# Performance work log

Measured on AMD Instinct MI355X. Metric: run time of the kernel, lower is better.

The kernel has to match this reference:

```python
import jax, jax.numpy as jnp
import numpy as np

HS, NH, HD = 768, 12, 64
MLP_DIM = 3072
WS = 14            # window size
B, H, W = 8, 64, 64
EPS = 1e-6


def _ln(x, g, b):
    mu = jnp.mean(x, axis=-1, keepdims=True)
    var = jnp.mean(jnp.square(x - mu), axis=-1, keepdims=True)
    return (x - mu) * jax.lax.rsqrt(var + EPS) * g + b


def setup_inputs() -> dict:
    key = jax.random.key(0)
    ks = jax.random.split(key, 8)
    s = 0.02
    return {
        "x": jax.random.normal(ks[0], (B, H, W, HS), dtype=jnp.float32),
        "ln1_g": jnp.ones((HS,), jnp.float32),
        "ln1_b": jnp.zeros((HS,), jnp.float32),
        "qkv_w": jax.random.normal(ks[1], (HS, 3 * HS), jnp.float32) * s,
        "qkv_b": jnp.zeros((3 * HS,), jnp.float32),
        "proj_w": jax.random.normal(ks[2], (HS, HS), jnp.float32) * s,
        "proj_b": jnp.zeros((HS,), jnp.float32),
        "rel_pos_h": jax.random.normal(ks[3], (2 * WS - 1, HD), jnp.float32) * s,
        "rel_pos_w": jax.random.normal(ks[4], (2 * WS - 1, HD), jnp.float32) * s,
        "ln2_g": jnp.ones((HS,), jnp.float32),
        "ln2_b": jnp.zeros((HS,), jnp.float32),
        "mlp_w1": jax.random.normal(ks[5], (HS, MLP_DIM), jnp.float32) * s,
        "mlp_b1": jnp.zeros((MLP_DIM,), jnp.float32),
        "mlp_w2": jax.random.normal(ks[6], (MLP_DIM, HS), jnp.float32) * s,
        "mlp_b2": jnp.zeros((HS,), jnp.float32),
    }


def reference(x, ln1_g, ln1_b, qkv_w, qkv_b, proj_w, proj_b,
              rel_pos_h, rel_pos_w, ln2_g, ln2_b,
              mlp_w1, mlp_b1, mlp_w2, mlp_b2):
    b, h, w, c = x.shape
    shortcut = x
    y = _ln(x, ln1_g, ln1_b)

    # ---- window partition (pad H,W to multiple of WS) ----
    pad = (-h) % WS
    hp = h + pad
    y = jnp.pad(y, ((0, 0), (0, pad), (0, pad), (0, 0)))
    n = hp // WS  # windows per side
    y = y.reshape(b, n, WS, n, WS, c).transpose(0, 1, 3, 2, 4, 5)
    y = y.reshape(b * n * n, WS, WS, c)          # (Bw, 14, 14, C)
    bw = y.shape[0]
    tok = WS * WS                                 # 196

    # ---- attention with decomposed relative position bias ----
    qkv = y.reshape(bw, tok, c) @ qkv_w + qkv_b   # (Bw, 196, 3C)
    qkv = qkv.reshape(bw, tok, 3, NH, HD).transpose(2, 0, 3, 1, 4)
    qkv = qkv.reshape(3, bw * NH, tok, HD)
    q, k, v = qkv[0], qkv[1], qkv[2]
    scale = HD ** -0.5
    attn = jnp.einsum('bqd,bkd->bqk', q * scale, k)  # (Bw*NH, 196, 196)

    idx = jnp.arange(WS)[:, None] - jnp.arange(WS)[None, :] + (WS - 1)
    Rh = rel_pos_h[idx]                            # (14, 14, HD)
    Rw = rel_pos_w[idx]                            # (14, 14, HD)
    qr = q.reshape(bw * NH, WS, WS, HD)
    rel_h = jnp.einsum('bhwc,hkc->bhwk', qr, Rh)   # (Bnh, h, w, k_h)
    rel_w = jnp.einsum('bhwc,wkc->bhwk', qr, Rw)   # (Bnh, h, w, k_w)
    bias = (rel_h[:, :, :, :, None] + rel_w[:, :, :, None, :])
    attn = attn + bias.reshape(bw * NH, tok, tok)

    attn = jax.nn.softmax(attn, axis=-1)
    out = jnp.einsum('bqk,bkd->bqd', attn, v)      # (Bw*NH, 196, HD)
    out = out.reshape(bw, NH, WS, WS, HD).transpose(0, 2, 3, 1, 4)
    out = out.reshape(bw, WS, WS, c) @ proj_w + proj_b

    # ---- window unpartition + crop ----
    out = out.reshape(b, n, n, WS, WS, c).transpose(0, 1, 3, 2, 4, 5)
    out = out.reshape(b, hp, hp, c)[:, :h, :w, :]

    x = shortcut + out

    # ---- MLP block ----
    y2 = _ln(x, ln2_g, ln2_b)
    y2 = jax.nn.gelu(y2 @ mlp_w1 + mlp_b1, approximate=False) @ mlp_w2 + mlp_b2
    return x + y2
```

## Files before the change

kernel.cpp:

```cpp
#include <hip/hip_runtime.h>
#include <hip/hip_bf16.h>
#include <math.h>


#define HS 768
#define NHEADS 12
#define HD 64
#define WSZ 14
#define TOK 196
#define HWDIM 64
#define NSIDE 5
#define WIN_PER_B 25

typedef __attribute__((ext_vector_type(8))) short short8;
typedef __attribute__((ext_vector_type(4))) float floatx4;
typedef __attribute__((ext_vector_type(4))) unsigned short ushort4v;

__device__ __forceinline__ float bf2f(unsigned short u) {
    union { unsigned int i; float f; } w; w.i = ((unsigned int)u) << 16; return w.f;
}
__device__ __forceinline__ unsigned short f2bu(float f) {
    __hip_bfloat16 h = __float2bfloat16(f);
    return *(unsigned short*)&h;
}

__device__ __forceinline__ void gload16(const void* g, void* l) {
    __builtin_amdgcn_global_load_lds(
        (const __attribute__((address_space(1))) void*)g,
        (__attribute__((address_space(3))) void*)l, 16, 0, 0);
}

__device__ __forceinline__ int gather_src(int m, int M, int win_base) {
    if (m >= M) return -1;
    int lwin = m / TOK, tok = m - lwin * TOK;
    int win = win_base + lwin;
    int bb = win / WIN_PER_B, r = win - bb * WIN_PER_B;
    int wi = r / NSIDE, wj = r - wi * NSIDE;
    int ti = tok / WSZ, tj = tok - ti * WSZ;
    int h = wi * WSZ + ti, w = wj * WSZ + tj;
    if (h < HWDIM && w < HWDIM) return (bb * HWDIM + h) * HWDIM + w;
    return -1;
}

__global__ __launch_bounds__(256)
void cvt_t_k(const float* __restrict__ src, __hip_bfloat16* __restrict__ dst,
             int K, int N) {
    __shared__ float t[32][33];
    int n0 = blockIdx.x * 32, k0 = blockIdx.y * 32;
    int tc = threadIdx.x & 31, tr8 = threadIdx.x >> 5;
    #pragma unroll
    for (int i = 0; i < 4; ++i) {
        int r = tr8 + i * 8;
        t[r][tc] = src[(size_t)(k0 + r) * N + n0 + tc];
    }
    __syncthreads();
    #pragma unroll
    for (int i = 0; i < 4; ++i) {
        int r = tr8 + i * 8;
        dst[(size_t)(n0 + r) * K + k0 + tc] = __float2bfloat16(t[tc][r]);
    }
}

__global__ __launch_bounds__(256)
void ln_k(const float* __restrict__ x, const float* __restrict__ g,
          const float* __restrict__ b, __hip_bfloat16* __restrict__ y) {
    int wave = threadIdx.x >> 6, lane = threadIdx.x & 63;
    int row = blockIdx.x * 4 + wave;
    const float4* xr = (const float4*)(x + (size_t)row * HS);
    float4 a0 = xr[lane], a1 = xr[lane + 64], a2 = xr[lane + 128];
    float s = a0.x + a0.y + a0.z + a0.w + a1.x + a1.y + a1.z + a1.w
            + a2.x + a2.y + a2.z + a2.w;
    float q = a0.x*a0.x + a0.y*a0.y + a0.z*a0.z + a0.w*a0.w
            + a1.x*a1.x + a1.y*a1.y + a1.z*a1.z + a1.w*a1.w
            + a2.x*a2.x + a2.y*a2.y + a2.z*a2.z + a2.w*a2.w;
    #pragma unroll
    for (int off = 32; off > 0; off >>= 1) {
        s += __shfl_down(s, off, 64);
        q += __shfl_down(q, off, 64);
    }
    s = __shfl(s, 0, 64);
    q = __shfl(q, 0, 64);
    float mu = s * (1.0f / HS);
    float var = q * (1.0f / HS) - mu * mu;
    float rstd = rsqrtf(var + 1e-6f);
    const float4* g4 = (const float4*)g;
    const float4* b4 = (const float4*)b;
    unsigned short* yr = (unsigned short*)y + (size_t)row * HS;
    float4 av[3] = {a0, a1, a2};
    #pragma unroll
    for (int c = 0; c < 3; ++c) {
        float4 gv = g4[lane + 64 * c], bv = b4[lane + 64 * c];
        float4 a = av[c];
        ushort4v o;
        o[0] = f2bu((a.x - mu) * rstd * gv.x + bv.x);
        o[1] = f2bu((a.y - mu) * rstd * gv.y + bv.y);
        o[2] = f2bu((a.z - mu) * rstd * gv.z + bv.z);
        o[3] = f2bu((a.w - mu) * rstd * gv.w + bv.w);
        *(ushort4v*)&yr[(lane + 64 * c) * 4] = o;
    }
}

template<int EP, int AGATHER, int BM, int BN, int KSPLIT>
__global__ __launch_bounds__(256, 4)
void gemm_k(const __hip_bfloat16* __restrict__ A,
            const __hip_bfloat16* __restrict__ Bt,
            const float* __restrict__ bias,
            int M, int N, int K,
            __hip_bfloat16* __restrict__ oq, __hip_bfloat16* __restrict__ okk,
            __hip_bfloat16* __restrict__ ov,
            float* __restrict__ of, const float* __restrict__ resid,
            __hip_bfloat16* __restrict__ oh,
            int win_base, int m_base)
{
    constexpr int LPW = (BM + BN) / 64;
    constexpr int FI = BM / 32;
    constexpr int FJ = BN / 32;
    constexpr int ASZ = BM * 32;
    constexpr int BSZ = BN * 32;
    __shared__ __align__(16) unsigned short lds[4 * (ASZ + BSZ)];
    unsigned short* Asb = lds;
    unsigned short* Bsb = lds + 4 * ASZ;

    int tid = threadIdx.x;
    int wave = tid >> 6, lane = tid & 63;
    int n16 = lane & 15, quad = lane >> 4;
    int wrr = wave >> 1, wcc = wave & 1;
    int bm = blockIdx.y * BM;
    int bn = blockIdx.x * BN;
    int kz = (KSPLIT > 1) ? blockIdx.z : 0;
    int kseg = K / KSPLIT;

    int srow = tid >> 2;
    int q4 = tid & 3;
    int skoff = (q4 ^ ((srow >> 1) & 3)) << 3;

    const unsigned short* Au = (const unsigned short*)A;
    const unsigned short* Bu = (const unsigned short*)Bt;

    int src0 = 0, src1 = 0;
    if (AGATHER) {
        int s0 = gather_src(bm + srow, M, win_base);
        src0 = s0 >= 0 ? s0 : 0;
        if (BM == 128) {
            int s1 = gather_src(bm + 64 + srow, M, win_base);
            src1 = s1 >= 0 ? s1 : 0;
        }
    } else {
        int m0 = bm + srow;
        src0 = m0 < M ? m0 : 0;
        if (BM == 128) { int m1 = bm + 64 + srow; src1 = m1 < M ? m1 : 0; }
    }

    const unsigned short* ap0 = Au + (size_t)src0 * K + kz * kseg + skoff;
    const unsigned short* ap1 = Au + (size_t)src1 * K + kz * kseg + skoff;
    const unsigned short* bp0 = Bu + (size_t)(bn + srow) * K + kz * kseg + skoff;
    const unsigned short* bp1 = Bu + (size_t)(bn + 64 + srow) * K + kz * kseg + skoff;

    auto stage = [&](int kt, int b) {
        size_t ko = (size_t)kt * 32;
        gload16(ap0 + ko, Asb + b * ASZ + wave * 512);
        if constexpr (BM == 128) gload16(ap1 + ko, Asb + b * ASZ + 2048 + wave * 512);
        gload16(bp0 + ko, Bsb + b * BSZ + wave * 512);
        if constexpr (BN == 128) gload16(bp1 + ko, Bsb + b * BSZ + 2048 + wave * 512);
    };

    floatx4 acc[FI][FJ] = {};
    int xr = (n16 >> 1) & 3;
    int nt = kseg >> 5;

    stage(0, 0);
    if (nt > 1) stage(1, 1);
    if (nt > 2) stage(2, 2);

    for (int t = 0; t < nt; ++t) {
        int cur = t & 3;
        int ahead = nt - 1 - t;
        if (ahead >= 2) {
            if constexpr (LPW == 4)      asm volatile("s_waitcnt vmcnt(8)" ::: "memory");
            else if constexpr (LPW == 3) asm volatile("s_waitcnt vmcnt(6)" ::: "memory");
            else                         asm volatile("s_waitcnt vmcnt(4)" ::: "memory");
        } else if (ahead == 1) {
            if constexpr (LPW == 4)      asm volatile("s_waitcnt vmcnt(4)" ::: "memory");
            else if constexpr (LPW == 3) asm volatile("s_waitcnt vmcnt(3)" ::: "memory");
            else                         asm volatile("s_waitcnt vmcnt(2)" ::: "memory");
        } else {
            asm volatile("s_waitcnt vmcnt(0)" ::: "memory");
        }
        __builtin_amdgcn_s_barrier();
        if (t + 3 < nt) stage(t + 3, (t + 3) & 3);
        short8 af[FI], bf[FJ];
        #pragma unroll
        for (int i = 0; i < FI; ++i) {
            int ra = wrr * (BM / 2) + i * 16 + n16;
            af[i] = *(const short8*)&Asb[cur * ASZ + ra * 32 + ((quad ^ xr) << 3)];
        }
        #pragma unroll
        for (int j = 0; j < FJ; ++j) {
            int rb = wcc * (BN / 2) + j * 16 + n16;
            bf[j] = *(const short8*)&Bsb[cur * BSZ + rb * 32 + ((quad ^ xr) << 3)];
        }
        #pragma unroll
        for (int i = 0; i < FI; ++i)
            #pragma unroll
            for (int j = 0; j < FJ; ++j)
                acc[i][j] = __builtin_amdgcn_mfma_f32_16x16x32_bf16(
                    af[i], bf[j], acc[i][j], 0, 0, 0);
        asm volatile("s_waitcnt lgkmcnt(0)" ::: "memory");
    }

    int rbase = bm + wrr * (BM / 2) + quad * 4;
    int cbase = bn + wcc * (BN / 2) + n16;

    if constexpr (EP == 0 || EP == 2) {
        constexpr int CLD = BN + 8;
        __syncthreads();
        unsigned short* Cs = lds;
        int ruseW[FI * 4];
        if (EP == 0) {
            #pragma unroll
            for (int i = 0; i < FI; ++i)
                #pragma unroll
                for (int r = 0; r < 4; ++r)
                    ruseW[i * 4 + r] = gather_src(rbase + i * 16 + r, M, win_base) >= 0;
        }
        #pragma unroll
        for (int j = 0; j < FJ; ++j) {
            int col_l = wcc * (BN / 2) + j * 16 + n16;
            float bcol = bias[bn + col_l];
            #pragma unroll
            for (int i = 0; i < FI; ++i) {
                #pragma unroll
                for (int r = 0; r < 4; ++r) {
                    int row_l = wrr * (BM / 2) + i * 16 + quad * 4 + r;
                    float val = acc[i][j][r] + bcol;
                    float vv;
                    if (EP == 0) {
                        vv = ruseW[i * 4 + r] ? val : bcol;
                    } else {
                        vv = 0.5f * val * (1.0f + erff(val * 0.70710678118654752f));
                    }
                    Cs[row_l * CLD + col_l] = f2bu(vv);
                }
            }
        }
        __syncthreads();
        #pragma unroll
        for (int rep = 0; rep < (BM * (BN / 64)) / 256; ++rep) {
            int idx = rep * 256 + tid;
            int row_l = idx / (BN / 64);
            int half = idx - row_l * (BN / 64);
            int m = bm + row_l;
            if (m < M) {
                unsigned short* srcu = &Cs[row_l * CLD + half * 64];
                unsigned short* dstu;
                if (EP == 0) {
                    int lwin = m / TOK, tok = m - lwin * TOK;
                    int colg = bn + half * 64;
                    int which = colg / HS;
                    int head = (colg - which * HS) >> 6;
                    __hip_bfloat16* dstp = (which == 0) ? oq : ((which == 1) ? okk : ov);
                    dstu = (unsigned short*)dstp +
                           ((size_t)(lwin * NHEADS + head) * TOK + tok) * HD;
                } else {
                    dstu = (unsigned short*)oh + (size_t)m * N + bn + half * 64;
                }
                #pragma unroll
                for (int s = 0; s < 8; ++s)
                    *(uint4*)(dstu + s * 8) = *(const uint4*)(srcu + s * 8);
            }
        }
    } else {
        int rowoff[FI * 4];
        int ruse[FI * 4];
        #pragma unroll
        for (int i = 0; i < FI; ++i) {
            #pragma unroll
            for (int r = 0; r < 4; ++r) {
                int ii = i * 4 + r;
                int row = rbase + i * 16 + r;
                if (EP == 1) {
                    int lwin = row / TOK, tok = row - lwin * TOK;
                    int win = win_base + lwin;
                    int bb = win / WIN_PER_B, rr2 = win - bb * WIN_PER_B;
                    int wi = rr2 / NSIDE, wj = rr2 - wi * NSIDE;
                    int ti = tok / WSZ, tj = tok - ti * WSZ;
                    int h = wi * WSZ + ti, w = wj * WSZ + tj;
                    ruse[ii] = (h < HWDIM) && (w < HWDIM);
                    rowoff[ii] = ((bb * HWDIM + h) * HWDIM + w) * HS;
                } else {
                    rowoff[ii] = (m_base + row) * HS;
                    ruse[ii] = 1;
                }
            }
        }
        #pragma unroll
        for (int j = 0; j < FJ; ++j) {
            int col = cbase + j * 16;
            float bcol = bias[col];
            if (EP == 3 && KSPLIT > 1 && kz != 0) bcol = 0.0f;
            #pragma unroll
            for (int i = 0; i < FI; ++i) {
                #pragma unroll
                for (int r = 0; r < 4; ++r) {
                    int ii = i * 4 + r;
                    int row = rbase + i * 16 + r;
                    if (row >= M) continue;
                    float val = acc[i][j][r] + bcol;
                    if (EP == 1) {
                        if (ruse[ii]) {
                            size_t idx = (size_t)rowoff[ii] + col;
                            of[idx] = resid[idx] + val;
                        }
                    } else {
                        size_t idx = (size_t)rowoff[ii] + col;
                        if (KSPLIT > 1) {
                            unsafeAtomicAdd(&of[idx], val);
                        } else {
                            of[idx] += val;
                        }
                    }
                }
            }
        }
    }
}

__global__ __launch_bounds__(256)
void attn_k(const __hip_bfloat16* __restrict__ qb, const __hip_bfloat16* __restrict__ kb,
            const __hip_bfloat16* __restrict__ vb,
            const float* __restrict__ rph, const float* __restrict__ rpw,
            __hip_bfloat16* __restrict__ ao)
{
    __shared__ __align__(16) unsigned short lds[32416];
    unsigned short* Ks = lds;
    unsigned short* Vt = lds + 14112;
    unsigned short* scr = lds + 28960;

    int bid = blockIdx.x;
    int lwin = bid / NHEADS, head = bid - lwin * NHEADS;
    size_t base = (size_t)(lwin * NHEADS + head) * TOK * HD;
    const unsigned short* q = (const unsigned short*)qb + base;
    const unsigned short* k = (const unsigned short*)kb + base;
    const unsigned short* v = (const unsigned short*)vb + base;

    int tid = threadIdx.x;
    int wave = tid >> 6, lane = tid & 63;
    int n16 = lane & 15, quad = lane >> 4;

    short8 btab[4][2];
    #pragma unroll
    for (int nt = 0; nt < 4; ++nt) {
        int n = nt * 16 + n16;
        #pragma unroll
        for (int kh = 0; kh < 2; ++kh) {
            short8 f = {0, 0, 0, 0, 0, 0, 0, 0};
            if (n < 54) {
                const float* src = (n < 27) ? (rph + (size_t)n * HD)
                                            : (rpw + (size_t)(n - 27) * HD);
                const float4* s4 = (const float4*)(src + kh * 32 + quad * 8);
                float4 a = s4[0], b = s4[1];
                f[0] = (short)f2bu(a.x); f[1] = (short)f2bu(a.y);
                f[2] = (short)f2bu(a.z); f[3] = (short)f2bu(a.w);
                f[4] = (short)f2bu(b.x); f[5] = (short)f2bu(b.y);
                f[6] = (short)f2bu(b.z); f[7] = (short)f2bu(b.w);
            }
            btab[nt][kh] = f;
        }
    }

    for (int idx = tid; idx < 1568; idx += 256) {
        int row = idx >> 3, q8 = (idx & 7) << 3;
        *(uint4*)&Ks[row * 72 + q8] = *(const uint4*)(k + (size_t)row * HD + q8);
    }
    for (int s = tid; s < 1568; s += 256) {
        int row = s >> 3, d8 = (s & 7) << 3;
        uint4 vv = *(const uint4*)(v + (size_t)row * HD + d8);
        const unsigned short* p = (const unsigned short*)&vv;
        #pragma unroll
        for (int e = 0; e < 8; ++e)
            Vt[(d8 + e) * 232 + row] = p[e];
    }
    for (int s = tid; s < 64 * 9; s += 256) {
        int r = s / 9, c = 196 + (s - r * 9) * 4;
        uint2 z = {0u, 0u};
        *(uint2*)&Vt[r * 232 + c] = z;
    }
    __syncthreads();

    unsigned short* myscr = &scr[wave * 864];
    int rl0 = quad * 4;

    for (int qt = wave; qt < 13; qt += 4) {
        int qrow = qt * 16 + n16;
        int qr = qrow < 196 ? qrow : 195;

        short8 qf0 = *(const short8*)(q + (size_t)qr * HD + quad * 8);
        short8 qf1 = *(const short8*)(q + (size_t)qr * HD + 32 + quad * 8);

        #pragma unroll
        for (int nt = 0; nt < 4; ++nt) {
            floatx4 cr = {0.f, 0.f, 0.f, 0.f};
            cr = __builtin_amdgcn_mfma_f32_16x16x32_bf16(qf0, btab[nt][0], cr, 0, 0, 0);
            cr = __builtin_amdgcn_mfma_f32_16x16x32_bf16(qf1, btab[nt][1], cr, 0, 0, 0);
            int c = nt * 16 + n16;
            if (c < 54) {
                #pragma unroll
                for (int r = 0; r < 4; ++r)
                    myscr[(rl0 + r) * 54 + c] = f2bu(cr[r]);
            }
        }

        floatx4 S[13];
        __builtin_amdgcn_s_setprio(1);
        #pragma unroll
        for (int nt = 0; nt < 13; ++nt) {
            short8 kf0 = *(const short8*)&Ks[(nt * 16 + n16) * 72 + quad * 8];
            short8 kf1 = *(const short8*)&Ks[(nt * 16 + n16) * 72 + 32 + quad * 8];
            floatx4 a = {0.f, 0.f, 0.f, 0.f};
            a = __builtin_amdgcn_mfma_f32_16x16x32_bf16(qf0, kf0, a, 0, 0, 0);
            a = __builtin_amdgcn_mfma_f32_16x16x32_bf16(qf1, kf1, a, 0, 0, 0);
            S[nt] = a;
        }
        __builtin_amdgcn_s_setprio(0);

        int ti4[4], tj4[4];
        #pragma unroll
        for (int r = 0; r < 4; ++r) {
            int grow = qt * 16 + rl0 + r;
            ti4[r] = grow / WSZ;
            tj4[r] = grow - ti4[r] * WSZ;
        }

        #pragma unroll
        for (int nt = 0; nt < 13; ++nt) {
            int col = nt * 16 + n16;
            int ki = col / WSZ, kj = col - ki * WSZ;
            #pragma unroll
            for (int r = 0; r < 4; ++r) {
                float rh = bf2f(myscr[(rl0 + r) * 54 + (ti4[r] - ki + 13)]);
                float rw = bf2f(myscr[(rl0 + r) * 54 + (40 + tj4[r] - kj)]);
                S[nt][r] = fmaf(S[nt][r], 0.125f, rh + rw);
            }
        }
        if (n16 >= 4) {
            #pragma unroll
            for (int r = 0; r < 4; ++r) S[12][r] = -1e30f;
        }

        float mxr[4] = {-3e30f, -3e30f, -3e30f, -3e30f};
        #pragma unroll
        for (int nt = 0; nt < 13; ++nt)
            #pragma unroll
            for (int r = 0; r < 4; ++r) mxr[r] = fmaxf(mxr[r], S[nt][r]);
        #pragma unroll
        for (int m = 1; m <= 8; m <<= 1)
            #pragma unroll
            for (int r = 0; r < 4; ++r) mxr[r] = fmaxf(mxr[r], __shfl_xor(mxr[r], m, 64));
        float sum[4] = {0.f, 0.f, 0.f, 0.f};
        #pragma unroll
        for (int nt = 0; nt < 13; ++nt)
            #pragma unroll
            for (int r = 0; r < 4; ++r) {
                float e = __expf(S[nt][r] - mxr[r]);
                S[nt][r] = e;
                sum[r] += e;
            }
        #pragma unroll
        for (int m = 1; m <= 8; m <<= 1)
            #pragma unroll
            for (int r = 0; r < 4; ++r) sum[r] += __shfl_xor(sum[r], m, 64);
        float inv[4];
        #pragma unroll
        for (int r = 0; r < 4; ++r) inv[r] = 1.0f / sum[r];

        floatx4 O[4] = {{0.f,0.f,0.f,0.f},{0.f,0.f,0.f,0.f},{0.f,0.f,0.f,0.f},{0.f,0.f,0.f,0.f}};
        __builtin_amdgcn_s_setprio(1);
        #pragma unroll
        for (int ks = 0; ks < 7; ++ks) {
            #pragma unroll
            for (int r = 0; r < 4; ++r) {
                myscr[(rl0 + r) * 40 + n16] = f2bu(S[2 * ks][r] * inv[r]);
                myscr[(rl0 + r) * 40 + 16 + n16] =
                    (2 * ks + 1 < 13) ? f2bu(S[2 * ks + 1][r] * inv[r]) : (unsigned short)0;
            }
            short8 pf = *(const short8*)&myscr[n16 * 40 + quad * 8];
            #pragma unroll
            for (int nt4 = 0; nt4 < 4; ++nt4) {
                short8 vf = *(const short8*)&Vt[(nt4 * 16 + n16) * 232 + ks * 32 + quad * 8];
                O[nt4] = __builtin_amdgcn_mfma_f32_16x16x32_bf16(pf, vf, O[nt4], 0, 0, 0);
            }
        }
        __builtin_amdgcn_s_setprio(0);

        #pragma unroll
        for (int nt4 = 0; nt4 < 4; ++nt4) {
            int d = nt4 * 16 + n16;
            #pragma unroll
            for (int r = 0; r < 4; ++r) {
                int row = qt * 16 + rl0 + r;
                if (row < 196) {
                    ao[((size_t)(lwin * TOK + row)) * HS + head * HD + d] =
                        __float2bfloat16(O[nt4][r]);
                }
            }
        }
    }
}

extern "C" void kernel_launch(void* const* d_in, const int* in_sizes, int n_in,
                              void* d_out, int out_size, void* d_ws, size_t ws_size,
                              hipStream_t stream)
{
    const float* x      = (const float*)d_in[0];
    const float* ln1_g  = (const float*)d_in[1];
    const float* ln1_b  = (const float*)d_in[2];
    const float* qkv_w  = (const float*)d_in[3];
    const float* qkv_b  = (const float*)d_in[4];
    const float* proj_w = (const float*)d_in[5];
    const float* proj_b = (const float*)d_in[6];
    const float* rph    = (const float*)d_in[7];
    const float* rpw    = (const float*)d_in[8];
    const float* ln2_g  = (const float*)d_in[9];
    const float* ln2_b  = (const float*)d_in[10];
    const float* mlp_w1 = (const float*)d_in[11];
    const float* mlp_b1 = (const float*)d_in[12];
    const float* mlp_w2 = (const float*)d_in[13];
    const float* mlp_b2 = (const float*)d_in[14];
    float* out = (float*)d_out;

    char* ws = (char*)d_ws;
    __hip_bfloat16* wqkv  = (__hip_bfloat16*)(ws + 0);
    __hip_bfloat16* wproj = (__hip_bfloat16*)(ws + 3538944);
    __hip_bfloat16* wm1   = (__hip_bfloat16*)(ws + 4718592);
    __hip_bfloat16* wm2   = (__hip_bfloat16*)(ws + 9437184);
    __hip_bfloat16* ybuf  = (__hip_bfloat16*)(ws + 14155776);
    char* R2 = ws + 64487424;
    __hip_bfloat16* hid = (__hip_bfloat16*)(R2);

    const size_t PERWIN = 301056;
    int nwin_chunk, nchunks;
    if (ws_size >= 64487424ull + 4ull * 200 * PERWIN) {
        nwin_chunk = 200; nchunks = 1;
    } else if (ws_size >= 64487424ull + 4ull * 100 * PERWIN) {
        nwin_chunk = 100; nchunks = 2;
    } else {
        nwin_chunk = 25; nchunks = 8;
    }
    size_t bufsz = (size_t)nwin_chunk * PERWIN;
    __hip_bfloat16* qc = (__hip_bfloat16*)(R2);
    __hip_bfloat16* kc = (__hip_bfloat16*)(R2 + bufsz);
    __hip_bfloat16* vc = (__hip_bfloat16*)(R2 + 2 * bufsz);
    __hip_bfloat16* ao = (__hip_bfloat16*)(R2 + 3 * bufsz);

    int mlpch, nmlp;
    if (ws_size >= 64487424ull + (size_t)16384 * 3072 * 2) {
        mlpch = 16384; nmlp = 2;
    } else {
        mlpch = 8192; nmlp = 4;
    }

    cvt_t_k<<<dim3(72, 24), 256, 0, stream>>>(qkv_w,  wqkv,  768, 2304);
    cvt_t_k<<<dim3(24, 24), 256, 0, stream>>>(proj_w, wproj, 768, 768);
    cvt_t_k<<<dim3(96, 24), 256, 0, stream>>>(mlp_w1, wm1,   768, 3072);
    cvt_t_k<<<dim3(24, 96), 256, 0, stream>>>(mlp_w2, wm2,  3072, 768);

    ln_k<<<dim3(8192), 256, 0, stream>>>(x, ln1_g, ln1_b, ybuf);

    for (int c = 0; c < nchunks; ++c) {
        int M = nwin_chunk * TOK;
        int wb = c * nwin_chunk;
        gemm_k<0, 1, 128, 128, 1><<<dim3(18, (M + 127) / 128), 256, 0, stream>>>(
            ybuf, wqkv, qkv_b, M, 2304, 768,
            qc, kc, vc, nullptr, nullptr, nullptr, wb, 0);
        attn_k<<<dim3(nwin_chunk * NHEADS), 256, 0, stream>>>(
            qc, kc, vc, rph, rpw, ao);
        gemm_k<1, 0, 128, 128, 1><<<dim3(6, (M + 127) / 128), 256, 0, stream>>>(
            ao, wproj, proj_b, M, 768, 768,
            nullptr, nullptr, nullptr, out, x, nullptr, wb, 0);
    }

    ln_k<<<dim3(8192), 256, 0, stream>>>(out, ln2_g, ln2_b, ybuf);

    for (int mc = 0; mc < nmlp; ++mc) {
        gemm_k<2, 0, 128, 128, 1><<<dim3(24, mlpch / 128), 256, 0, stream>>>(
            ybuf + (size_t)mc * mlpch * HS, wm1, mlp_b1, mlpch, 3072, 768,
            nullptr, nullptr, nullptr, nullptr, nullptr, hid, 0, 0);
        gemm_k<3, 0, 128, 64, 1><<<dim3(12, mlpch / 128), 256, 0, stream>>>(
            hid, wm2, mlp_b2, mlpch, 768, 3072,
            nullptr, nullptr, nullptr, out, nullptr, nullptr, 0, mc * mlpch);
    }
}
```

Before: 1.516 ms.

## Fold relative-position bias into QK MFMA via one-hot key extension

Adds a third MFMA per key tile, multiplying a per-query vector of gathered rel_h/rel_w values by a one-hot key-index matrix held in LDS. This removes the per-element scalar LDS gathers and FMAs that previously added the bias to scores. The 0.125 scale is pre-applied to q, and the relative tables are pre-multiplied by 8 so the bias comes out unscaled. In exchange it costs extra LDS, an extra bf16 rounding of q and of the bias, and one more MFMA per tile.

```diff
diff --git a/kernel.cpp b/kernel.cpp
--- a/kernel.cpp
+++ b/kernel.cpp
@@ -331,10 +331,11 @@
             const float* __restrict__ rph, const float* __restrict__ rpw,
             __hip_bfloat16* __restrict__ ao)
 {
-    __shared__ __align__(16) unsigned short lds[32416];
+    __shared__ __align__(16) unsigned short lds[40736];
     unsigned short* Ks = lds;
     unsigned short* Vt = lds + 14112;
-    unsigned short* scr = lds + 28960;
+    unsigned short* KE = lds + 28960;
+    unsigned short* scr = lds + 37280;
 
     int bid = blockIdx.x;
     int lwin = bid / NHEADS, head = bid - lwin * NHEADS;
@@ -359,10 +360,10 @@
                                             : (rpw + (size_t)(n - 27) * HD);
                 const float4* s4 = (const float4*)(src + kh * 32 + quad * 8);
                 float4 a = s4[0], b = s4[1];
-                f[0] = (short)f2bu(a.x); f[1] = (short)f2bu(a.y);
-                f[2] = (short)f2bu(a.z); f[3] = (short)f2bu(a.w);
-                f[4] = (short)f2bu(b.x); f[5] = (short)f2bu(b.y);
-                f[6] = (short)f2bu(b.z); f[7] = (short)f2bu(b.w);
+                f[0] = (short)f2bu(a.x * 8.0f); f[1] = (short)f2bu(a.y * 8.0f);
+                f[2] = (short)f2bu(a.z * 8.0f); f[3] = (short)f2bu(a.w * 8.0f);
+                f[4] = (short)f2bu(b.x * 8.0f); f[5] = (short)f2bu(b.y * 8.0f);
+                f[6] = (short)f2bu(b.z * 8.0f); f[7] = (short)f2bu(b.w * 8.0f);
             }
             btab[nt][kh] = f;
         }
@@ -385,6 +386,16 @@
         uint2 z = {0u, 0u};
         *(uint2*)&Vt[r * 232 + c] = z;
     }
+    for (int krow = tid; krow < 208; krow += 256) {
+        int ki = krow / WSZ, kj = krow - ki * WSZ;
+        int valid = krow < TOK;
+        #pragma unroll
+        for (int c = 0; c < 32; ++c) {
+            unsigned short vv = 0;
+            if (valid && (c == ki || c == 14 + kj)) vv = 0x3F80;
+            KE[krow * 40 + c] = vv;
+        }
+    }
     __syncthreads();
 
     unsigned short* myscr = &scr[wave * 864];
@@ -394,8 +405,14 @@
         int qrow = qt * 16 + n16;
         int qr = qrow < 196 ? qrow : 195;
 
-        short8 qf0 = *(const short8*)(q + (size_t)qr * HD + quad * 8);
-        short8 qf1 = *(const short8*)(q + (size_t)qr * HD + 32 + quad * 8);
+        short8 raw0 = *(const short8*)(q + (size_t)qr * HD + quad * 8);
+        short8 raw1 = *(const short8*)(q + (size_t)qr * HD + 32 + quad * 8);
+        short8 qf0, qf1;
+        #pragma unroll
+        for (int e = 0; e < 8; ++e) {
+            qf0[e] = (short)f2bu(bf2f((unsigned short)raw0[e]) * 0.125f);
+            qf1[e] = (short)f2bu(bf2f((unsigned short)raw1[e]) * 0.125f);
+        }
 
         #pragma unroll
         for (int nt = 0; nt < 4; ++nt) {
@@ -410,38 +427,34 @@
             }
         }
 
+        int ti_l = qr / WSZ, tj_l = qr - ti_l * WSZ;
+        short8 qf2;
+        #pragma unroll
+        for (int e = 0; e < 8; ++e) {
+            int d = quad * 8 + e;
+            int idx_i = n16 * 54 + ti_l + 13 - d;
+            int idx_j = n16 * 54 + 40 + tj_l - (d - 14);
+            int idx = (d < 14) ? idx_i : idx_j;
+            unsigned short vv = (d < 28) ? myscr[idx] : (unsigned short)0;
+            qf2[e] = (short)vv;
+        }
+
         floatx4 S[13];
         __builtin_amdgcn_s_setprio(1);
         #pragma unroll
         for (int nt = 0; nt < 13; ++nt) {
-            short8 kf0 = *(const short8*)&Ks[(nt * 16 + n16) * 72 + quad * 8];
-            short8 kf1 = *(const short8*)&Ks[(nt * 16 + n16) * 72 + 32 + quad * 8];
+            int kr = nt * 16 + n16;
+            short8 kf0 = *(const short8*)&Ks[kr * 72 + quad * 8];
+            short8 kf1 = *(const short8*)&Ks[kr * 72 + 32 + quad * 8];
+            short8 kf2 = *(const short8*)&KE[kr * 40 + quad * 8];
             floatx4 a = {0.f, 0.f, 0.f, 0.f};
             a = __builtin_amdgcn_mfma_f32_16x16x32_bf16(qf0, kf0, a, 0, 0, 0);
             a = __builtin_amdgcn_mfma_f32_16x16x32_bf16(qf1, kf1, a, 0, 0, 0);
+            a = __builtin_amdgcn_mfma_f32_16x16x32_bf16(qf2, kf2, a, 0, 0, 0);
             S[nt] = a;
         }
         __builtin_amdgcn_s_setprio(0);
 
-        int ti4[4], tj4[4];
-        #pragma unroll
-        for (int r = 0; r < 4; ++r) {
-            int grow = qt * 16 + rl0 + r;
-            ti4[r] = grow / WSZ;
-            tj4[r] = grow - ti4[r] * WSZ;
-        }
-
-        #pragma unroll
-        for (int nt = 0; nt < 13; ++nt) {
-            int col = nt * 16 + n16;
-            int ki = col / WSZ, kj = col - ki * WSZ;
-            #pragma unroll
-            for (int r = 0; r < 4; ++r) {
-                float rh = bf2f(myscr[(rl0 + r) * 54 + (ti4[r] - ki + 13)]);
-                float rw = bf2f(myscr[(rl0 + r) * 54 + (40 + tj4[r] - kj)]);
-                S[nt][r] = fmaf(S[nt][r], 0.125f, rh + rw);
-            }
-        }
         if (n16 >= 4) {
             #pragma unroll
             for (int r = 0; r < 4; ++r) S[12][r] = -1e30f;
```

Result: faster. 1.415 ms (-6.7%).
